# Optimization experiments

Measured on AMD Instinct MI355X. Metric: run time of the kernel, lower is better.

Reference implementation:

```python
import jax, jax.numpy as jnp
import numpy as np

GROUPS = 32
EPS = 1e-5


def group_norm(x, weight, bias):
    # x: [B, C, H, W]; normalize per (group, H, W) as torch nn.GroupNorm
    B, C, H, W = x.shape
    xg = x.reshape(B, GROUPS, C // GROUPS, H, W)
    mean = xg.mean(axis=(2, 3, 4), keepdims=True)
    var = xg.var(axis=(2, 3, 4), keepdims=True)
    xg = (xg - mean) * jax.lax.rsqrt(var + EPS)
    x = xg.reshape(B, C, H, W)
    return x * weight[None, :, None, None] + bias[None, :, None, None]


def setup_inputs() -> dict:
    key = jax.random.key(0)
    ks = jax.random.split(key, 8)
    B, C, H, W = 2, 512, 64, 64
    s = 1.0 / np.sqrt(C)  # linear-init-like scale to keep logits sane
    return {
        "x": jax.random.normal(ks[0], (B, C, H, W), dtype=jnp.float32),
        "gn_weight": jnp.ones((C,), jnp.float32),
        "gn_bias": jnp.zeros((C,), jnp.float32),
        "wq": jax.random.normal(ks[1], (C, C), jnp.float32) * s,
        "bq": jnp.zeros((C,), jnp.float32),
        "wk": jax.random.normal(ks[2], (C, C), jnp.float32) * s,
        "bk": jnp.zeros((C,), jnp.float32),
        "wv": jax.random.normal(ks[3], (C, C), jnp.float32) * s,
        "bv": jnp.zeros((C,), jnp.float32),
        "wo": jax.random.normal(ks[4], (C, C), jnp.float32) * s,
        "bo": jnp.zeros((C,), jnp.float32),
    }


def reference(x, gn_weight, gn_bias, wq, bq, wk, bk, wv, bv, wo, bo):
    B, C, H, W = x.shape
    residual = x
    h = group_norm(x, gn_weight, gn_bias)
    # [B, N, C] tokens, N = H*W
    t = h.reshape(B, C, H * W).transpose(0, 2, 1)
    q = t @ wq.T + bq
    k = t @ wk.T + bk
    v = t @ wv.T + bv
    scale = C ** (-0.5)
    # naive full attention: [B, N, N]
    attn = jax.nn.softmax(jnp.einsum("bnc,bmc->bnm", q, k) * scale, axis=-1)
    out = jnp.einsum("bnm,bmc->bnc", attn, v)
    out = out @ wo.T + bo
    out = out.transpose(0, 2, 1).reshape(B, C, H, W)
    return out + residual
```

## Files before the change

kernel.cpp:

```cpp
#include <hip/hip_runtime.h>
#include <cstddef>
#include <cstdint>


typedef __attribute__((ext_vector_type(8))) short frag8;
typedef __attribute__((ext_vector_type(4))) float f32x4;

#define GLOAD16(g, l)                                                        \
    __builtin_amdgcn_global_load_lds(                                        \
        (const __attribute__((address_space(1))) void*)(g),                  \
        (__attribute__((address_space(3))) void*)(l), 16, 0, 0)

__device__ __forceinline__ float b2f(unsigned short u) {
    union { unsigned u32; float f; } v; v.u32 = ((unsigned)u) << 16; return v.f;
}
__device__ __forceinline__ unsigned short f2bu(float f) {
    unsigned u = __float_as_uint(f);
    unsigned r = u + 0x7fffu + ((u >> 16) & 1u);
    return (unsigned short)(r >> 16);
}

__global__ __launch_bounds__(256) void cast_f32_bf16(const float* __restrict__ src,
                                                     unsigned short* __restrict__ dst,
                                                     int n) {
    int i = (blockIdx.x * 256 + threadIdx.x) * 8;
    if (i >= n) return;
    float4 a = *reinterpret_cast<const float4*>(src + i);
    float4 b = *reinterpret_cast<const float4*>(src + i + 4);
    float vv[8] = {a.x, a.y, a.z, a.w, b.x, b.y, b.z, b.w};
    union { unsigned short u16[8]; uint4 v; } o;
#pragma unroll
    for (int j = 0; j < 8; ++j) o.u16[j] = f2bu(vv[j]);
    *reinterpret_cast<uint4*>(dst + i) = o.v;
}

__global__ __launch_bounds__(256) void gn_stats(const float* __restrict__ x,
                                                float* __restrict__ stats) {
    const int tid = threadIdx.x;
    const float* p = x + (size_t)blockIdx.x * 65536;
    float s = 0.f, ss = 0.f;
    for (int i = tid * 8; i < 65536; i += 2048) {
        float4 a = *reinterpret_cast<const float4*>(p + i);
        float4 b = *reinterpret_cast<const float4*>(p + i + 4);
        float vv[8] = {a.x, a.y, a.z, a.w, b.x, b.y, b.z, b.w};
#pragma unroll
        for (int j = 0; j < 8; ++j) { s += vv[j]; ss += vv[j] * vv[j]; }
    }
#pragma unroll
    for (int o = 32; o; o >>= 1) { s += __shfl_xor(s, o, 64); ss += __shfl_xor(ss, o, 64); }
    __shared__ float rs[4], rss[4];
    int wv = tid >> 6, lane = tid & 63;
    if (lane == 0) { rs[wv] = s; rss[wv] = ss; }
    __syncthreads();
    if (tid == 0) {
        float S1 = rs[0] + rs[1] + rs[2] + rs[3];
        float S2 = rss[0] + rss[1] + rss[2] + rss[3];
        float mean = S1 * (1.f / 65536.f);
        float var  = fmaxf(S2 * (1.f / 65536.f) - mean * mean, 0.f);
        stats[blockIdx.x * 2 + 0] = mean;
        stats[blockIdx.x * 2 + 1] = rsqrtf(var + 1e-5f);
    }
}

__global__ __launch_bounds__(256) void build_t(const float* __restrict__ x,
                                               const float* __restrict__ stats,
                                               const float* __restrict__ gnw,
                                               const float* __restrict__ gnb,
                                               unsigned short* __restrict__ t) {
    __shared__ unsigned short tile[64 * 66];
    const int b = blockIdx.z, c0 = blockIdx.y * 64, hw0 = blockIdx.x * 64;
#pragma unroll
    for (int it = 0; it < 2; ++it) {
        int idx = it * 256 + threadIdx.x;
        int c = idx >> 3, v8 = idx & 7;
        int cg = c0 + c;
        int g = cg >> 4;
        float mean = stats[(b * 32 + g) * 2 + 0];
        float rstd = stats[(b * 32 + g) * 2 + 1];
        float sc = rstd * gnw[cg];
        float sh = gnb[cg] - mean * sc;
        const float* src = x + ((size_t)(b * 512 + cg)) * 4096 + hw0 + v8 * 8;
        float4 a = *reinterpret_cast<const float4*>(src);
        float4 bb = *reinterpret_cast<const float4*>(src + 4);
        float vv[8] = {a.x, a.y, a.z, a.w, bb.x, bb.y, bb.z, bb.w};
#pragma unroll
        for (int j = 0; j < 8; ++j)
            tile[c * 66 + v8 * 8 + j] = f2bu(vv[j] * sc + sh);
    }
    __syncthreads();
#pragma unroll
    for (int it = 0; it < 2; ++it) {
        int idx = it * 256 + threadIdx.x;
        int hw = idx >> 3, v8 = idx & 7;
        union { unsigned short u16[8]; uint4 v; } outv;
#pragma unroll
        for (int j = 0; j < 8; ++j) outv.u16[j] = tile[(v8 * 8 + j) * 66 + hw];
        *reinterpret_cast<uint4*>(t + ((size_t)(b * 4096 + hw0 + hw)) * 512 + c0 + v8 * 8) =
            outv.v;
    }
}

template <int MODE>
__global__ __launch_bounds__(256) void gemm_bt(const unsigned short* __restrict__ A,
                                               const unsigned short* __restrict__ B,
                                               const unsigned short* __restrict__ bias,
                                               const float* __restrict__ resid,
                                               unsigned short* __restrict__ C,
                                               float* __restrict__ Cf,
                                               int M, int N, int K, float alpha,
                                               size_t zA, size_t zB, size_t zC) {
    __shared__ __attribute__((aligned(16))) unsigned short As[128 * 32];
    __shared__ __attribute__((aligned(16))) unsigned short Bs[128 * 32];

    A += (size_t)blockIdx.z * zA;
    B += (size_t)blockIdx.z * zB;
    C += (size_t)blockIdx.z * zC;

    const int tid = threadIdx.x;
    const int lane = tid & 63, wv = tid >> 6;
    const int lrow = lane & 15, quad = lane >> 4;
    const int wr = (wv & 1) * 64, wc = (wv >> 1) * 64;

    const unsigned short* Ag = A + ((size_t)blockIdx.x * 128 + wv * 16 + (lane >> 2)) * K + (lane & 3) * 8;
    const unsigned short* Bg = B + ((size_t)blockIdx.y * 128 + wv * 16 + (lane >> 2)) * K + (lane & 3) * 8;
    unsigned short* Asw = As + wv * 512;
    unsigned short* Bsw = Bs + wv * 512;
    const size_t rowskip = (size_t)64 * K;

    f32x4 acc[4][4] = {};

    for (int k0 = 0; k0 < K; k0 += 32) {
        GLOAD16(Ag + k0,           Asw);
        GLOAD16(Ag + k0 + rowskip, Asw + 2048);
        GLOAD16(Bg + k0,           Bsw);
        GLOAD16(Bg + k0 + rowskip, Bsw + 2048);
        __syncthreads();

        frag8 af[4], bf[4];
        const unsigned short* ap = As + (wr + lrow) * 32 + quad * 8;
        const unsigned short* bp = Bs + (wc + lrow) * 32 + quad * 8;
#pragma unroll
        for (int i = 0; i < 4; ++i) af[i] = *reinterpret_cast<const frag8*>(ap + i * 512);
#pragma unroll
        for (int j = 0; j < 4; ++j) bf[j] = *reinterpret_cast<const frag8*>(bp + j * 512);
#pragma unroll
        for (int i = 0; i < 4; ++i)
#pragma unroll
            for (int j = 0; j < 4; ++j)
                acc[i][j] = __builtin_amdgcn_mfma_f32_16x16x32_bf16(af[i], bf[j], acc[i][j], 0, 0, 0);
        __syncthreads();
    }

    const int rowBase = blockIdx.x * 128 + wr + quad * 4;
    const int colBase = blockIdx.y * 128 + wc + lrow;
#pragma unroll
    for (int j = 0; j < 4; ++j) {
        const int col = colBase + j * 16;
        float badd = 0.f;
        if (MODE == 3 && bias) badd = b2f(bias[col]);
#pragma unroll
        for (int i = 0; i < 4; ++i) {
            const int row = rowBase + i * 16;
#pragma unroll
            for (int r = 0; r < 4; ++r) {
                const int rr = row + r;
                float v = acc[i][j][r];
                if (MODE == 2) v *= alpha;
                v += badd;
                if (MODE == 2) {
                    C[(size_t)rr * N + col] = f2bu(v);
                } else {
                    size_t addr = ((size_t)(rr >> 12) * 512 + col) * 4096 + (rr & 4095);
                    Cf[addr] = v + resid[addr];
                }
            }
        }
    }
}

__global__ __launch_bounds__(256) void gemm_qkv(const unsigned short* __restrict__ A,
                                                const unsigned short* __restrict__ Ball,
                                                const unsigned short* __restrict__ biasAll,
                                                unsigned short* __restrict__ q,
                                                unsigned short* __restrict__ k,
                                                unsigned short* __restrict__ vT) {
    __shared__ __attribute__((aligned(16))) unsigned short As[128 * 32];
    __shared__ __attribute__((aligned(16))) unsigned short Bs[128 * 32];
    const int K = 512;

    const int tid = threadIdx.x;
    const int lane = tid & 63, wv = tid >> 6;
    const int lrow = lane & 15, quad = lane >> 4;
    const int wr = (wv & 1) * 64, wc = (wv >> 1) * 64;

    const unsigned short* B = Ball + (size_t)blockIdx.y * 128 * 512;
    const unsigned short* Ag = A + ((size_t)blockIdx.x * 128 + wv * 16 + (lane >> 2)) * K + (lane & 3) * 8;
    const unsigned short* Bg = B + ((size_t)(wv * 16 + (lane >> 2))) * K + (lane & 3) * 8;
    unsigned short* Asw = As + wv * 512;
    unsigned short* Bsw = Bs + wv * 512;
    const size_t rowskip = (size_t)64 * K;

    f32x4 acc[4][4] = {};

    for (int k0 = 0; k0 < K; k0 += 32) {
        GLOAD16(Ag + k0,           Asw);
        GLOAD16(Ag + k0 + rowskip, Asw + 2048);
        GLOAD16(Bg + k0,           Bsw);
        GLOAD16(Bg + k0 + rowskip, Bsw + 2048);
        __syncthreads();

        frag8 af[4], bf[4];
        const unsigned short* ap = As + (wr + lrow) * 32 + quad * 8;
        const unsigned short* bp = Bs + (wc + lrow) * 32 + quad * 8;
#pragma unroll
        for (int i = 0; i < 4; ++i) af[i] = *reinterpret_cast<const frag8*>(ap + i * 512);
#pragma unroll
        for (int j = 0; j < 4; ++j) bf[j] = *reinterpret_cast<const frag8*>(bp + j * 512);
#pragma unroll
        for (int i = 0; i < 4; ++i)
#pragma unroll
            for (int j = 0; j < 4; ++j)
                acc[i][j] = __builtin_amdgcn_mfma_f32_16x16x32_bf16(af[i], bf[j], acc[i][j], 0, 0, 0);
        __syncthreads();
    }

    const int rowBase = blockIdx.x * 128 + wr + quad * 4;
    const int colBase = wc + lrow;
    const int gbase = blockIdx.y * 128;
#pragma unroll
    for (int j = 0; j < 4; ++j) {
        const int colL = colBase + j * 16;
        const int gcol = gbase + colL;
        const float badd = b2f(biasAll[gcol]);
#pragma unroll
        for (int i = 0; i < 4; ++i) {
            const int row = rowBase + i * 16;
#pragma unroll
            for (int r = 0; r < 4; ++r) {
                const int rr = row + r;
                float v = acc[i][j][r] + badd;
                if (blockIdx.y < 4) {
                    q[(size_t)rr * 512 + gcol] = f2bu(v);
                } else if (blockIdx.y < 8) {
                    k[(size_t)rr * 512 + (gcol - 512)] = f2bu(v);
                } else {
                    int ch = gcol - 1024;
                    vT[((size_t)(rr >> 12) * 512 + ch) * 4096 + (rr & 4095)] = f2bu(v);
                }
            }
        }
    }
}

__global__ __launch_bounds__(512, 2) void pv_gemm(const unsigned short* __restrict__ S0,
                                                  const unsigned short* __restrict__ vT0,
                                                  unsigned short* __restrict__ O0) {
    __shared__ __attribute__((aligned(16))) unsigned short As[4 * 4096];
    __shared__ __attribute__((aligned(16))) unsigned short Bs[4 * 4096];

    const int tid = threadIdx.x;
    const int lane = tid & 63, wv = tid >> 6;
    const int lrow = lane & 15, quad = lane >> 4;
    const int wm = wv & 1, wn = wv >> 1;
    const int z = blockIdx.z;

    const unsigned short* A = S0 + (size_t)z * 16777216;
    const unsigned short* B = vT0 + (size_t)z * 2097152;
    unsigned short* C = O0 + (size_t)z * 2097152;

    const int srow = (tid >> 6) * 16 + ((tid & 63) >> 2);
    const unsigned short* Ag = A + ((size_t)blockIdx.x * 128 + srow) * 4096 + (tid & 3) * 8;
    const unsigned short* Bg = B + ((size_t)blockIdx.y * 128 + srow) * 4096 + (tid & 3) * 8;
    unsigned short* Asw = As + wv * 512;
    unsigned short* Bsw = Bs + wv * 512;

    f32x4 acc[4][2] = {};

    for (int k0 = 0; k0 < 4096; k0 += 128) {
#pragma unroll
        for (int i = 0; i < 4; ++i) {
            GLOAD16(Ag + k0 + i * 32, Asw + i * 4096);
            GLOAD16(Bg + k0 + i * 32, Bsw + i * 4096);
        }
        __syncthreads();

#pragma unroll
        for (int kk = 0; kk < 4; ++kk) {
            const unsigned short* ap = As + kk * 4096 + (wm * 64 + lrow) * 32 + quad * 8;
            const unsigned short* bp = Bs + kk * 4096 + (wn * 32 + lrow) * 32 + quad * 8;
            frag8 af[4], bf[2];
#pragma unroll
            for (int i = 0; i < 4; ++i) af[i] = *reinterpret_cast<const frag8*>(ap + i * 512);
#pragma unroll
            for (int j = 0; j < 2; ++j) bf[j] = *reinterpret_cast<const frag8*>(bp + j * 512);
#pragma unroll
            for (int i = 0; i < 4; ++i)
#pragma unroll
                for (int j = 0; j < 2; ++j)
                    acc[i][j] = __builtin_amdgcn_mfma_f32_16x16x32_bf16(af[i], bf[j], acc[i][j], 0, 0, 0);
        }
        __syncthreads();
    }

    const int rowBase = blockIdx.x * 128 + wm * 64 + quad * 4;
    const int colBase = blockIdx.y * 128 + wn * 32 + lrow;
#pragma unroll
    for (int j = 0; j < 2; ++j) {
        const int col = colBase + j * 16;
#pragma unroll
        for (int i = 0; i < 4; ++i) {
            const int row = rowBase + i * 16;
#pragma unroll
            for (int r = 0; r < 4; ++r)
                C[(size_t)(row + r) * 512 + col] = f2bu(acc[i][j][r]);
        }
    }
}

__global__ __launch_bounds__(512, 2) void ksplit_o(const unsigned short* __restrict__ A,
                                                   const unsigned short* __restrict__ B,
                                                   unsigned short* __restrict__ C,
                                                   int N, int K) {
    __shared__ __attribute__((aligned(16))) unsigned char smem[65536];
    const int tid = threadIdx.x;
    const int lane = tid & 63, wv = tid >> 6;
    const int lrow = lane & 15, quad = lane >> 4;
    const int colhalf = wv & 1;
    const int kz = wv >> 1;
    const int Kw = K >> 2;
    const int yt = blockIdx.x;
    const int xt = blockIdx.y;

    unsigned short* Aw = (unsigned short*)smem + wv * 4096;
    unsigned short* Bw = Aw + 2048;

    const unsigned short* Ag = A + ((size_t)xt * 64 + (lane >> 2)) * K + kz * Kw + (lane & 3) * 8;
    const unsigned short* Bg = B + ((size_t)(yt * 128 + colhalf * 64 + (lane >> 2))) * K + kz * Kw + (lane & 3) * 8;
    const size_t rowskip16 = (size_t)16 * K;

    f32x4 acc[4][4] = {};

    for (int k0 = 0; k0 < Kw; k0 += 32) {
        uint4 av[4], bv_[4];
#pragma unroll
        for (int i = 0; i < 4; ++i) {
            av[i]  = *reinterpret_cast<const uint4*>(Ag + k0 + i * rowskip16);
            bv_[i] = *reinterpret_cast<const uint4*>(Bg + k0 + i * rowskip16);
        }
#pragma unroll
        for (int i = 0; i < 4; ++i) {
            *reinterpret_cast<uint4*>(Aw + i * 512 + lane * 8) = av[i];
            *reinterpret_cast<uint4*>(Bw + i * 512 + lane * 8) = bv_[i];
        }
        frag8 af[4], bf[4];
#pragma unroll
        for (int i = 0; i < 4; ++i) {
            af[i] = *reinterpret_cast<const frag8*>(Aw + i * 512 + lrow * 32 + quad * 8);
            bf[i] = *reinterpret_cast<const frag8*>(Bw + i * 512 + lrow * 32 + quad * 8);
        }
        __builtin_amdgcn_s_setprio(1);
#pragma unroll
        for (int i = 0; i < 4; ++i)
#pragma unroll
            for (int j = 0; j < 4; ++j)
                acc[i][j] = __builtin_amdgcn_mfma_f32_16x16x32_bf16(af[i], bf[j], acc[i][j], 0, 0, 0);
        __builtin_amdgcn_s_setprio(0);
    }

    __syncthreads();
    float* fbase = (float*)smem;
    if (kz == 0 || kz == 2) {
        float* f = fbase + (colhalf * 2 + (kz >> 1)) * 4096;
#pragma unroll
        for (int i = 0; i < 4; ++i)
#pragma unroll
            for (int j = 0; j < 4; ++j)
#pragma unroll
                for (int r = 0; r < 4; ++r)
                    f[(i * 16 + quad * 4 + r) * 64 + j * 16 + lrow] = acc[i][j][r];
    }
    __syncthreads();
    if (kz == 1 || kz == 3) {
        float* f = fbase + (colhalf * 2 + (kz >> 1)) * 4096;
#pragma unroll
        for (int i = 0; i < 4; ++i)
#pragma unroll
            for (int j = 0; j < 4; ++j)
#pragma unroll
                for (int r = 0; r < 4; ++r)
                    f[(i * 16 + quad * 4 + r) * 64 + j * 16 + lrow] += acc[i][j][r];
    }
    __syncthreads();
#pragma unroll
    for (int e = 0; e < 16; ++e) {
        int idx = e * 512 + tid;
        int row = idx >> 7, colL = idx & 127;
        int ch = colL >> 6, c = colL & 63;
        float v = fbase[(ch * 2 + 0) * 4096 + row * 64 + c] +
                  fbase[(ch * 2 + 1) * 4096 + row * 64 + c];
        C[((size_t)xt * 64 + row) * N + yt * 128 + colL] = f2bu(v);
    }
}

__global__ __launch_bounds__(256) void softmax_rows(unsigned short* __restrict__ S) {
    __shared__ float red[8];
    const int tid = threadIdx.x;
    const int wv = tid >> 6, lane = tid & 63;
    unsigned short* p = S + (size_t)blockIdx.x * 4096 + tid * 16;

    uint4 r0 = *reinterpret_cast<const uint4*>(p);
    uint4 r1 = *reinterpret_cast<const uint4*>(p + 8);
    unsigned w[8] = {r0.x, r0.y, r0.z, r0.w, r1.x, r1.y, r1.z, r1.w};
    float v[16];
#pragma unroll
    for (int q2 = 0; q2 < 8; ++q2) {
        v[q2 * 2 + 0] = b2f((unsigned short)(w[q2] & 0xffffu));
        v[q2 * 2 + 1] = b2f((unsigned short)(w[q2] >> 16));
    }
    float m = -3.0e38f;
#pragma unroll
    for (int q2 = 0; q2 < 16; ++q2) m = fmaxf(m, v[q2]);
#pragma unroll
    for (int o = 32; o; o >>= 1) m = fmaxf(m, __shfl_xor(m, o, 64));
    if (lane == 0) red[wv] = m;
    __syncthreads();
    m = fmaxf(fmaxf(red[0], red[1]), fmaxf(red[2], red[3]));

    float s = 0.f;
#pragma unroll
    for (int q2 = 0; q2 < 16; ++q2) { v[q2] = __expf(v[q2] - m); s += v[q2]; }
#pragma unroll
    for (int o = 32; o; o >>= 1) s += __shfl_xor(s, o, 64);
    if (lane == 0) red[4 + wv] = s;
    __syncthreads();
    s = red[4] + red[5] + red[6] + red[7];
    const float inv = 1.f / s;

    unsigned ow[8];
#pragma unroll
    for (int q2 = 0; q2 < 8; ++q2) {
        unsigned lo = f2bu(v[q2 * 2 + 0] * inv);
        unsigned hi = f2bu(v[q2 * 2 + 1] * inv);
        ow[q2] = lo | (hi << 16);
    }
    uint4 o0 = {ow[0], ow[1], ow[2], ow[3]};
    uint4 o1 = {ow[4], ow[5], ow[6], ow[7]};
    *reinterpret_cast<uint4*>(p) = o0;
    *reinterpret_cast<uint4*>(p + 8) = o1;
}

__global__ void write_sentinel_f32(float* out, float code) {
    if (threadIdx.x == 0) out[0] = code;
}

extern "C" void kernel_launch(void* const* d_in, const int* in_sizes, int n_in,
                              void* d_out, int out_size, void* d_ws, size_t ws_size,
                              hipStream_t stream) {
    const float* x   = (const float*)d_in[0];
    const float* gnw = (const float*)d_in[1];
    const float* gnb = (const float*)d_in[2];
    const float* wq  = (const float*)d_in[3];
    const float* bq  = (const float*)d_in[4];
    const float* wk  = (const float*)d_in[5];
    const float* bk  = (const float*)d_in[6];
    const float* wv  = (const float*)d_in[7];
    const float* bv  = (const float*)d_in[8];
    const float* wo  = (const float*)d_in[9];
    const float* bo  = (const float*)d_in[10];
    float* out = (float*)d_out;

    bool shapes_ok = (n_in == 11 && in_sizes[0] == 4194304 && in_sizes[1] == 512 &&
                      in_sizes[3] == 262144 && out_size == 4194304);
    size_t half = ws_size / 2;
    if (!shapes_ok || half < (size_t)17831936 + 128 * 4096) {
        write_sentinel_f32<<<1, 64, 0, stream>>>(out, shapes_ok ? 8000.f : 9000.f);
        return;
    }

    unsigned short* ws = (unsigned short*)d_ws;
    unsigned short* t  = ws;
    unsigned short* q  = ws + 4194304;
    unsigned short* k  = ws + 8388608;
    unsigned short* vT = ws + 12582912;
    unsigned short* o  = t;
    const float scale = 0.044194173824159216f;

    unsigned short* wB0 = ws + 16777216;
    unsigned short* wB3 = ws + 17563648;
    unsigned short* bB0 = ws + 17825792;
    unsigned short* bB3 = ws + 17827328;
    float* stats = (float*)(ws + 17827840);

    cast_f32_bf16<<<128, 256, 0, stream>>>(wq, wB0,          262144);
    cast_f32_bf16<<<128, 256, 0, stream>>>(wk, wB0 + 262144, 262144);
    cast_f32_bf16<<<128, 256, 0, stream>>>(wv, wB0 + 524288, 262144);
    cast_f32_bf16<<<1, 256, 0, stream>>>(bq, bB0,        512);
    cast_f32_bf16<<<1, 256, 0, stream>>>(bk, bB0 + 512,  512);
    cast_f32_bf16<<<1, 256, 0, stream>>>(bv, bB0 + 1024, 512);

    gn_stats<<<64, 256, 0, stream>>>(x, stats);
    build_t<<<dim3(64, 8, 2), 256, 0, stream>>>(x, stats, gnw, gnb, t);
    gemm_qkv<<<dim3(64, 12), 256, 0, stream>>>(t, wB0, bB0, q, k, vT);

    if (half >= (size_t)50331648) {
        unsigned short* S = ws + 16777216;
        gemm_bt<2><<<dim3(32, 32, 2), 256, 0, stream>>>(q, k, nullptr, nullptr, S, nullptr,
                                                        4096, 4096, 512, scale,
                                                        2097152, 2097152, 16777216);
        softmax_rows<<<8192, 256, 0, stream>>>(S);
        pv_gemm<<<dim3(32, 4, 2), 512, 0, stream>>>(S, vT, o);
    } else if (half >= (size_t)33554432) {
        unsigned short* S = ws + 16777216;
        for (int b = 0; b < 2; ++b) {
            const unsigned short* qb  = q  + (size_t)b * 2097152;
            const unsigned short* kb  = k  + (size_t)b * 2097152;
            const unsigned short* vTb = vT + (size_t)b * 2097152;
            unsigned short*       ob  = o  + (size_t)b * 2097152;
            gemm_bt<2><<<dim3(32, 32), 256, 0, stream>>>(qb, kb, nullptr, nullptr, S, nullptr,
                                                         4096, 4096, 512, scale, 0, 0, 0);
            softmax_rows<<<4096, 256, 0, stream>>>(S);
            ksplit_o<<<dim3(4, 64), 512, 0, stream>>>(S, vTb, ob, 512, 4096);
        }
    } else {
        unsigned short* S = ws + 17831936;
        size_t avail = half - 17831936;
        int R = 4096;
        while (R > 128 && (size_t)R * 4096 > avail) R >>= 1;
        for (int b = 0; b < 2; ++b) {
            const unsigned short* qb  = q  + (size_t)b * 2097152;
            const unsigned short* kb  = k  + (size_t)b * 2097152;
            const unsigned short* vTb = vT + (size_t)b * 2097152;
            unsigned short*       ob  = o  + (size_t)b * 2097152;
            for (int r0 = 0; r0 < 4096; r0 += R) {
                gemm_bt<2><<<dim3(R / 128, 32), 256, 0, stream>>>(
                    qb + (size_t)r0 * 512, kb, nullptr, nullptr, S, nullptr, R, 4096, 512, scale,
                    0, 0, 0);
                softmax_rows<<<R, 256, 0, stream>>>(S);
                ksplit_o<<<dim3(4, R / 64), 512, 0, stream>>>(
                    S, vTb, ob + (size_t)r0 * 512, 512, 4096);
            }
        }
    }
    cast_f32_bf16<<<128, 256, 0, stream>>>(wo, wB3, 262144);
    cast_f32_bf16<<<1, 256, 0, stream>>>(bo, bB3, 512);
    gemm_bt<3><<<dim3(64, 4), 256, 0, stream>>>(o, wB3, bB3, x, nullptr, out,
                                                8192, 512, 512, 1.f, 0, 0, 0);
}
```

Before: 296.8 us.

## Double-buffer pv_gemm LDS tiles with XOR-swizzled layout to overlap loads and MFMA

Rewrites the P·V GEMM main loop to use two LDS buffers of 128x64 tiles, prefetching the next k-tile with global_load_lds while computing the current one, with a single barrier per iteration instead of two. The LDS layout is changed to 64-element rows with an XOR swizzle on 16-byte chunks to reduce bank conflicts on fragment reads. Launch bounds drop to one block per CU hint, trading occupancy for latency hiding via explicit software pipelining.

New measurement: 290.2 us. 2.2% less time.

```diff
diff --git a/kernel.cpp b/kernel.cpp
--- a/kernel.cpp
+++ b/kernel.cpp
@@ -252,67 +252,94 @@
     }
 }
 
-__global__ __launch_bounds__(512, 2) void pv_gemm(const unsigned short* __restrict__ S0,
+__global__ __launch_bounds__(512, 1) void pv_gemm(const unsigned short* __restrict__ S0,
                                                   const unsigned short* __restrict__ vT0,
                                                   unsigned short* __restrict__ O0) {
-    __shared__ __attribute__((aligned(16))) unsigned short As[4 * 4096];
-    __shared__ __attribute__((aligned(16))) unsigned short Bs[4 * 4096];
+    __shared__ __attribute__((aligned(16))) unsigned short Ab[2][8192];
+    __shared__ __attribute__((aligned(16))) unsigned short Bb[2][8192];
 
     const int tid = threadIdx.x;
-    const int lane = tid & 63, wv = tid >> 6;
+    const int lane = tid & 63, w = tid >> 6;
     const int lrow = lane & 15, quad = lane >> 4;
-    const int wm = wv & 1, wn = wv >> 1;
+    const int wm = w & 1, wn = w >> 1;
     const int z = blockIdx.z;
 
     const unsigned short* A = S0 + (size_t)z * 16777216;
     const unsigned short* B = vT0 + (size_t)z * 2097152;
     unsigned short* C = O0 + (size_t)z * 2097152;
 
-    const int srow = (tid >> 6) * 16 + ((tid & 63) >> 2);
-    const unsigned short* Ag = A + ((size_t)blockIdx.x * 128 + srow) * 4096 + (tid & 3) * 8;
-    const unsigned short* Bg = B + ((size_t)blockIdx.y * 128 + srow) * 4096 + (tid & 3) * 8;
-    unsigned short* Asw = As + wv * 512;
-    unsigned short* Bsw = Bs + wv * 512;
+    const int srow = w * 8 + (lane >> 3);
+    const int skc  = ((lane & 7) ^ (lane >> 3)) * 8;
+    const unsigned short* Ag = A + ((size_t)blockIdx.x * 128 + srow) * 4096 + skc;
+    const unsigned short* Bg = B + ((size_t)blockIdx.y * 128 + srow) * 4096 + skc;
+    const size_t rowskip64 = (size_t)64 * 4096;
 
     f32x4 acc[4][2] = {};
 
-    for (int k0 = 0; k0 < 4096; k0 += 128) {
-#pragma unroll
-        for (int i = 0; i < 4; ++i) {
-            GLOAD16(Ag + k0 + i * 32, Asw + i * 4096);
-            GLOAD16(Bg + k0 + i * 32, Bsw + i * 4096);
-        }
-        __syncthreads();
-
-#pragma unroll
-        for (int kk = 0; kk < 4; ++kk) {
-            const unsigned short* ap = As + kk * 4096 + (wm * 64 + lrow) * 32 + quad * 8;
-            const unsigned short* bp = Bs + kk * 4096 + (wn * 32 + lrow) * 32 + quad * 8;
-            frag8 af[4], bf[2];
-#pragma unroll
-            for (int i = 0; i < 4; ++i) af[i] = *reinterpret_cast<const frag8*>(ap + i * 512);
-#pragma unroll
-            for (int j = 0; j < 2; ++j) bf[j] = *reinterpret_cast<const frag8*>(bp + j * 512);
-#pragma unroll
-            for (int i = 0; i < 4; ++i)
-#pragma unroll
-                for (int j = 0; j < 2; ++j)
-                    acc[i][j] = __builtin_amdgcn_mfma_f32_16x16x32_bf16(af[i], bf[j], acc[i][j], 0, 0, 0);
-        }
-        __syncthreads();
-    }
+#define PV_STAGE(cur, kt)                                                    \
+    do {                                                                     \
+        const unsigned short* a_ = Ag + (size_t)(kt) * 64;                   \
+        const unsigned short* b_ = Bg + (size_t)(kt) * 64;                   \
+        GLOAD16(a_,            &Ab[cur][w * 512]);                           \
+        GLOAD16(a_ + rowskip64, &Ab[cur][4096 + w * 512]);                   \
+        GLOAD16(b_,            &Bb[cur][w * 512]);                           \
+        GLOAD16(b_ + rowskip64, &Bb[cur][4096 + w * 512]);                   \
+    } while (0)
+
+#define PV_COMPUTE(cur)                                                      \
+    do {                                                                     \
+        const int rbA = (wm * 64 + lrow) * 64;                               \
+        const int rbB = (wn * 32 + lrow) * 64;                               \
+        _Pragma("unroll")                                                    \
+        for (int kk = 0; kk < 2; ++kk) {                                     \
+            const int us = (((kk * 4 + quad) ^ (lrow & 7)) * 8);             \
+            frag8 af[4], bf[2];                                              \
+            _Pragma("unroll")                                                \
+            for (int i = 0; i < 4; ++i)                                      \
+                af[i] = *reinterpret_cast<const frag8*>(&Ab[cur][rbA + i * 1024 + us]); \
+            _Pragma("unroll")                                                \
+            for (int j2 = 0; j2 < 2; ++j2)                                   \
+                bf[j2] = *reinterpret_cast<const frag8*>(&Bb[cur][rbB + j2 * 1024 + us]); \
+            _Pragma("unroll")                                                \
+            for (int i = 0; i < 4; ++i)                                      \
+                _Pragma("unroll")                                            \
+                for (int j2 = 0; j2 < 2; ++j2)                               \
+                    acc[i][j2] = __builtin_amdgcn_mfma_f32_16x16x32_bf16(    \
+                        af[i], bf[j2], acc[i][j2], 0, 0, 0);                 \
+        }                                                                    \
+    } while (0)
+
+    PV_STAGE(0, 0);
+    asm volatile("s_waitcnt vmcnt(0)" ::: "memory");
+    __builtin_amdgcn_s_barrier();
+    __builtin_amdgcn_sched_barrier(0);
+
+    int cur = 0;
+    for (int kt = 0; kt < 63; ++kt) {
+        PV_STAGE(cur ^ 1, kt + 1);
+        __builtin_amdgcn_sched_barrier(0);
+        PV_COMPUTE(cur);
+        asm volatile("s_waitcnt vmcnt(0)" ::: "memory");
+        __builtin_amdgcn_s_barrier();
+        __builtin_amdgcn_sched_barrier(0);
+        cur ^= 1;
+    }
+    PV_COMPUTE(cur);
+
+#undef PV_STAGE
+#undef PV_COMPUTE
 
     const int rowBase = blockIdx.x * 128 + wm * 64 + quad * 4;
     const int colBase = blockIdx.y * 128 + wn * 32 + lrow;
 #pragma unroll
-    for (int j = 0; j < 2; ++j) {
-        const int col = colBase + j * 16;
+    for (int j2 = 0; j2 < 2; ++j2) {
+        const int col = colBase + j2 * 16;
 #pragma unroll
         for (int i = 0; i < 4; ++i) {
             const int row = rowBase + i * 16;
 #pragma unroll
             for (int r = 0; r < 4; ++r)
-                C[(size_t)(row + r) * 512 + col] = f2bu(acc[i][j][r]);
+                C[(size_t)(row + r) * 512 + col] = f2bu(acc[i][j2][r]);
         }
     }
 }
```
